# Kernel tuning notes

Measured on AMD Instinct MI355X. Metric: run time of the kernel, lower is better.

The kernel has to match this reference:

```python
import jax, jax.numpy as jnp
import numpy as np

B, S, D = 2, 2048, 2048
H = 16
HD = D // H

def setup_inputs() -> dict:
    key = jax.random.key(0)
    ks = jax.random.split(key, 6)
    s = 1.0 / np.sqrt(D)
    return {
        "inputs": jax.random.normal(ks[0], (B, S, D), dtype=jnp.float32),
        "w_q": jax.random.normal(ks[1], (D, D), dtype=jnp.float32) * s,
        "w_k": jax.random.normal(ks[2], (D, D), dtype=jnp.float32) * s,
        "w_v": jax.random.normal(ks[3], (D, D), dtype=jnp.float32) * s,
        "w_o": jax.random.normal(ks[4], (D, D), dtype=jnp.float32) * s,
        "b_o": jax.random.normal(ks[5], (D,), dtype=jnp.float32) * 0.02,
    }

def reference(inputs, w_q, w_k, w_v, w_o, b_o):
    b, t, _ = inputs.shape
    # Linear layers: y = x @ W^T (weights stored torch-style [out, in])
    q = (inputs @ w_q.T).reshape(b, t, H, HD)
    k = (inputs @ w_k.T).reshape(b, t, H, HD)
    v = (inputs @ w_v.T).reshape(b, t, H, HD)
    # scores: [b, h, t, t]
    scores = jnp.einsum('bqhd,bkhd->bhqk', q, k)
    causal = jnp.triu(jnp.ones((t, t), dtype=bool), k=1)
    scores = jnp.where(causal, -jnp.inf, scores)
    # NOTE: source scales by sqrt(token_num) (keys.shape[2] after transpose), not sqrt(head_dim)
    scale = jnp.float32(t) ** 0.5
    attn = jax.nn.softmax(scores / scale, axis=-1)
    ctx = jnp.einsum('bhqk,bkhd->bqhd', attn, v).reshape(b, t, D)
    return ctx @ w_o.T + b_o
```

## Files before the change

### kernel.cpp

```cpp
#include <hip/hip_runtime.h>


typedef __attribute__((ext_vector_type(8))) short short8;
typedef __attribute__((ext_vector_type(4))) float f32x4;

#define SEQ 2048
#define DM  2048
#define NHD 128
#define NT  32
#define QSCALE (0.022097086912079608f * 1.4426950408889634f)

#define EXP2F(x) __builtin_amdgcn_exp2f(x)
#define WAITV(N) asm volatile("s_waitcnt vmcnt(" #N ")" ::: "memory")

__device__ __forceinline__ unsigned short f2bf(float f) {
  unsigned u = __builtin_bit_cast(unsigned, f);
  u += 0x7FFFu + ((u >> 16) & 1u);
  return (unsigned short)(u >> 16);
}
__device__ __forceinline__ unsigned short f2bf_fast(float f) {
  unsigned u = __builtin_bit_cast(unsigned, f);
  return (unsigned short)((u + 0x8000u) >> 16);
}

__device__ __forceinline__ void gll16(const void* g, void* l) {
  __builtin_amdgcn_global_load_lds((const __attribute__((address_space(1))) void*)g,
                                   (__attribute__((address_space(3))) void*)l, 16, 0, 0);
}

template <int CTRL>
__device__ __forceinline__ float dpp_mv(float x) {
  int xi = __builtin_bit_cast(int, x);
  return __builtin_bit_cast(float,
      __builtin_amdgcn_update_dpp(xi, xi, CTRL, 0xF, 0xF, false));
}
__device__ __forceinline__ float red16_max(float x) {
  x = fmaxf(x, dpp_mv<0xB1>(x));
  x = fmaxf(x, dpp_mv<0x4E>(x));
  x = fmaxf(x, dpp_mv<0x124>(x));
  x = fmaxf(x, dpp_mv<0x128>(x));
  return x;
}
__device__ __forceinline__ float red16_sum(float x) {
  x += dpp_mv<0xB1>(x);
  x += dpp_mv<0x4E>(x);
  x += dpp_mv<0x124>(x);
  x += dpp_mv<0x128>(x);
  return x;
}

__global__ __launch_bounds__(256) void cast_all_k(const float* __restrict__ X,
                                                  const float* __restrict__ Wq,
                                                  const float* __restrict__ Wk,
                                                  const float* __restrict__ Wv,
                                                  const float* __restrict__ Wo,
                                                  unsigned short* __restrict__ Xb,
                                                  unsigned short* __restrict__ Wqb,
                                                  unsigned short* __restrict__ Wkb,
                                                  unsigned short* __restrict__ Wvb,
                                                  unsigned short* __restrict__ Wob) {
  int i = blockIdx.x * 256 + threadIdx.x;
  const float* src;
  unsigned short* dst;
  int j;
  float sc = 1.0f;
  if (i < 1048576) {
    src = X; dst = Xb; j = i;
  } else {
    int k = i - 1048576;
    int r = k >> 19; j = k & 524287;
    src = (r == 0) ? Wq : (r == 1) ? Wk : (r == 2) ? Wv : Wo;
    dst = (r == 0) ? Wqb : (r == 1) ? Wkb : (r == 2) ? Wvb : Wob;
    if (r == 0) sc = QSCALE;
  }
  const f32x4* p = (const f32x4*)src + (size_t)j * 2;
  f32x4 a = p[0], b = p[1];
  short8 o;
  o[0] = (short)f2bf(a[0] * sc); o[1] = (short)f2bf(a[1] * sc);
  o[2] = (short)f2bf(a[2] * sc); o[3] = (short)f2bf(a[3] * sc);
  o[4] = (short)f2bf(b[0] * sc); o[5] = (short)f2bf(b[1] * sc);
  o[6] = (short)f2bf(b[2] * sc); o[7] = (short)f2bf(b[3] * sc);
  *(short8*)(dst + (size_t)j * 8) = o;
}

__device__ __forceinline__ void stage_half(const unsigned short* __restrict__ gbase,
                                           unsigned short* lhalf, int tid) {
#pragma unroll
  for (int c = 0; c < 2; ++c) {
    int G = c * 512 + tid;
    int row = G >> 3, g = G & 7;
    int gs = g ^ (row & 7);
    gll16(gbase + (size_t)row * DM + gs * 8, lhalf + (size_t)G * 8);
  }
}

#define LOADAF(MH)                                                              \
  _Pragma("unroll") for (int mi = 0; mi < 4; ++mi)                              \
    _Pragma("unroll") for (int ks = 0; ks < 2; ++ks) {                          \
      int row = wm * 64 + mi * 16 + lr;                                         \
      af[mi][ks] = *(const short8*)&lA[(MH) * 8192 + row * 64 +                 \
                                       (((ks * 4 + kb) ^ (row & 7)) * 8)];      \
    }

#define PHASE(MH, NH, STG, WV)                                                  \
  {                                                                             \
    const unsigned short* lBh = lB + (NH) * 8192;                               \
    short8 bfr[2][2];                                                           \
    _Pragma("unroll") for (int ni = 0; ni < 2; ++ni)                            \
      _Pragma("unroll") for (int ks = 0; ks < 2; ++ks) {                        \
        int row = wn * 32 + ni * 16 + lr;                                       \
        bfr[ni][ks] = *(const short8*)&lBh[row * 64 + (((ks * 4 + kb) ^ (row & 7)) * 8)]; \
      }                                                                         \
    STG;                                                                        \
    __builtin_amdgcn_s_barrier();                                               \
    __builtin_amdgcn_s_setprio(1);                                              \
    _Pragma("unroll") for (int mi = 0; mi < 4; ++mi)                            \
      _Pragma("unroll") for (int ni = 0; ni < 2; ++ni) {                        \
        acc[MH][NH][mi][ni] = __builtin_amdgcn_mfma_f32_16x16x32_bf16(          \
            af[mi][0], bfr[ni][0], acc[MH][NH][mi][ni], 0, 0, 0);               \
        acc[MH][NH][mi][ni] = __builtin_amdgcn_mfma_f32_16x16x32_bf16(          \
            af[mi][1], bfr[ni][1], acc[MH][NH][mi][ni], 0, 0, 0);               \
      }                                                                         \
    __builtin_amdgcn_s_setprio(0);                                              \
    WV;                                                                         \
    __builtin_amdgcn_s_barrier();                                               \
  }

__device__ __forceinline__ void gemm256_core(const unsigned short* __restrict__ A,
                                             const unsigned short* __restrict__ B,
                                             unsigned short* LA, unsigned short* LB,
                                             f32x4 acc[2][2][4][2], int m0, int n0) {
  const int tid = threadIdx.x;
  const int w = tid >> 6, l = tid & 63;
  const int lr = l & 15, kb = l >> 4;
  const int wm = w >> 2, wn = w & 3;

  stage_half(A + (size_t)m0 * DM, LA, tid);
  stage_half(B + (size_t)n0 * DM, LB, tid);
  stage_half(B + (size_t)n0 * DM + (size_t)128 * DM, LB + 8192, tid);
  stage_half(A + (size_t)m0 * DM + (size_t)128 * DM, LA + 8192, tid);
  WAITV(4);
  __builtin_amdgcn_s_barrier();

#pragma unroll 1
  for (int t = 0; t < NT; ++t) {
    const unsigned short* lA = LA + (t & 1) * 16384;
    const unsigned short* lB = LB + (t & 1) * 16384;
    unsigned short* sA = LA + ((t + 1) & 1) * 16384;
    unsigned short* sB = LB + ((t + 1) & 1) * 16384;
    const unsigned short* gA = A + (size_t)m0 * DM + (t + 1) * 64;
    const unsigned short* gB = B + (size_t)n0 * DM + (t + 1) * 64;
    const bool st = (t + 1 < NT);
    short8 af[4][2];
    LOADAF(0);
    PHASE(0, 0, if (st) stage_half(gA, sA, tid),
                if (st) { WAITV(4); } else { WAITV(2); });
    PHASE(0, 1, if (st) stage_half(gB, sB, tid),
                if (st) { WAITV(4); } else { WAITV(0); });
    LOADAF(1);
    PHASE(1, 0, if (st) stage_half(gB + (size_t)128 * DM, sB + 8192, tid), );
    PHASE(1, 1, if (st) stage_half(gA + (size_t)128 * DM, sA + 8192, tid),
                if (st) { WAITV(4); });
  }
}

__global__ __launch_bounds__(512, 2) void gemm_qk_k(const unsigned short* __restrict__ X,
                                                    const unsigned short* __restrict__ Wq,
                                                    const unsigned short* __restrict__ Wk,
                                                    unsigned short* __restrict__ Qo,
                                                    unsigned short* __restrict__ Ko) {
  __shared__ unsigned short LA[32768];
  __shared__ unsigned short LB[32768];
  const int lin = blockIdx.x + 8 * (blockIdx.y + 16 * blockIdx.z);
  const int c = lin & 7, idx = lin >> 3;
  const int xb = (c & 1) * 4 + ((idx >> 2) & 3);
  const int yb = (c >> 1) * 4 + (idx & 3);
  const int zb = idx >> 4;
  const unsigned short* W = zb ? Wk : Wq;
  unsigned short* Y = zb ? Ko : Qo;
  const int m0 = yb * 256, n0 = xb * 256;
  const int tid = threadIdx.x, w = tid >> 6, l = tid & 63;
  const int lr = l & 15, kb = l >> 4;
  const int wm = w >> 2, wn = w & 3;
  f32x4 acc[2][2][4][2] = {};
  gemm256_core(X, W, LA, LB, acc, m0, n0);
#pragma unroll
  for (int mh = 0; mh < 2; ++mh)
#pragma unroll
    for (int nh = 0; nh < 2; ++nh)
#pragma unroll
      for (int mi = 0; mi < 4; ++mi)
#pragma unroll
        for (int ni = 0; ni < 2; ++ni)
#pragma unroll
          for (int rr = 0; rr < 4; ++rr) {
            int row = m0 + mh * 128 + wm * 64 + mi * 16 + kb * 4 + rr;
            int col = n0 + nh * 128 + wn * 32 + ni * 16 + lr;
            Y[(size_t)row * DM + col] = f2bf(acc[mh][nh][mi][ni][rr]);
          }
}

#define PH2(NH, STG, WV)                                                        \
  {                                                                             \
    const unsigned short* lBh = lB + (NH) * 8192;                               \
    short8 bfr[2][2];                                                           \
    _Pragma("unroll") for (int ni = 0; ni < 2; ++ni)                            \
      _Pragma("unroll") for (int ks = 0; ks < 2; ++ks) {                        \
        int row = wn * 32 + ni * 16 + lr;                                       \
        bfr[ni][ks] = *(const short8*)&lBh[row * 64 + (((ks * 4 + kb) ^ (row & 7)) * 8)]; \
      }                                                                         \
    STG;                                                                        \
    __builtin_amdgcn_s_barrier();                                               \
    __builtin_amdgcn_s_setprio(1);                                              \
    _Pragma("unroll") for (int mi = 0; mi < 4; ++mi)                            \
      _Pragma("unroll") for (int ni = 0; ni < 2; ++ni) {                        \
        acc[NH][mi][ni] = __builtin_amdgcn_mfma_f32_16x16x32_bf16(              \
            af[mi][0], bfr[ni][0], acc[NH][mi][ni], 0, 0, 0);                   \
        acc[NH][mi][ni] = __builtin_amdgcn_mfma_f32_16x16x32_bf16(              \
            af[mi][1], bfr[ni][1], acc[NH][mi][ni], 0, 0, 0);                   \
      }                                                                         \
    __builtin_amdgcn_s_setprio(0);                                              \
    WV;                                                                         \
    __builtin_amdgcn_s_barrier();                                               \
  }

__device__ __forceinline__ void gemm128x256_core(const unsigned short* __restrict__ A,
                                                 const unsigned short* __restrict__ B,
                                                 unsigned short* LA, unsigned short* LB,
                                                 f32x4 acc[2][4][2], int m0, int n0) {
  const int tid = threadIdx.x;
  const int w = tid >> 6, l = tid & 63;
  const int lr = l & 15, kb = l >> 4;
  const int wm = w >> 2, wn = w & 3;

  stage_half(A + (size_t)m0 * DM, LA, tid);
  stage_half(B + (size_t)n0 * DM, LB, tid);
  stage_half(B + (size_t)n0 * DM + (size_t)128 * DM, LB + 8192, tid);
  WAITV(2);
  __builtin_amdgcn_s_barrier();

#pragma unroll 1
  for (int t = 0; t < NT; ++t) {
    const unsigned short* lA = LA + (t & 1) * 8192;
    const unsigned short* lB = LB + (t & 1) * 16384;
    unsigned short* sA = LA + ((t + 1) & 1) * 8192;
    unsigned short* sB = LB + ((t + 1) & 1) * 16384;
    const unsigned short* gA = A + (size_t)m0 * DM + (t + 1) * 64;
    const unsigned short* gB = B + (size_t)n0 * DM + (t + 1) * 64;
    const bool st = (t + 1 < NT);
    short8 af[4][2];
#pragma unroll
    for (int mi = 0; mi < 4; ++mi)
#pragma unroll
      for (int ks = 0; ks < 2; ++ks) {
        int row = wm * 64 + mi * 16 + lr;
        af[mi][ks] = *(const short8*)&lA[row * 64 + (((ks * 4 + kb) ^ (row & 7)) * 8)];
      }
    PH2(0, if (st) stage_half(gA, sA, tid),
           if (st) { WAITV(2); } else { WAITV(0); });
    PH2(1, if (st) { stage_half(gB, sB, tid); stage_half(gB + (size_t)128 * DM, sB + 8192, tid); },
           if (st) { WAITV(2); });
  }
}

__global__ __launch_bounds__(512, 2) void gemm_vt_k(const unsigned short* __restrict__ Wv,
                                                    const unsigned short* __restrict__ X,
                                                    unsigned short* __restrict__ Vt) {
  __shared__ unsigned short LA[16384];
  __shared__ unsigned short LB[32768];
  const int lin = blockIdx.x + 16 * blockIdx.y;
  const int c = lin & 7, idx = lin >> 3;
  const int yb = (c >> 2) * 8 + (idx & 7);
  const int xb = (c & 3) * 4 + (idx >> 3);
  const int m0 = yb * 128, n0 = xb * 256;
  const int tid = threadIdx.x, w = tid >> 6, l = tid & 63;
  const int lr = l & 15, kb = l >> 4;
  const int wm = w >> 2, wn = w & 3;
  f32x4 acc[2][4][2] = {};
  gemm128x256_core(Wv, X, LA, LB, acc, m0, n0);
#pragma unroll
  for (int nh = 0; nh < 2; ++nh)
#pragma unroll
    for (int mi = 0; mi < 4; ++mi)
#pragma unroll
      for (int ni = 0; ni < 2; ++ni)
#pragma unroll
        for (int rr = 0; rr < 4; ++rr) {
          int i = m0 + wm * 64 + mi * 16 + kb * 4 + rr;
          int j = n0 + nh * 128 + wn * 32 + ni * 16 + lr;
          Vt[((size_t)(j >> 11) * 2048 + i) * 2048 + (j & 2047)] = f2bf(acc[nh][mi][ni][rr]);
        }
}

__global__ __launch_bounds__(512, 2) void gemm_o_k(const unsigned short* __restrict__ A,
                                                   const unsigned short* __restrict__ W,
                                                   const float* __restrict__ bias,
                                                   float* __restrict__ Y) {
  __shared__ unsigned short LA[16384];
  __shared__ unsigned short LB[32768];
  const int lin = blockIdx.x + 8 * blockIdx.y;
  const int c = lin & 7, idx = lin >> 3;
  const int yb = (c >> 1) * 8 + (idx & 7);
  const int xb = (c & 1) * 4 + (idx >> 3);
  const int m0 = yb * 128, n0 = xb * 256;
  const int tid = threadIdx.x, w = tid >> 6, l = tid & 63;
  const int lr = l & 15, kb = l >> 4;
  const int wm = w >> 2, wn = w & 3;
  f32x4 acc[2][4][2] = {};
  gemm128x256_core(A, W, LA, LB, acc, m0, n0);
#pragma unroll
  for (int nh = 0; nh < 2; ++nh)
#pragma unroll
    for (int mi = 0; mi < 4; ++mi)
#pragma unroll
      for (int ni = 0; ni < 2; ++ni)
#pragma unroll
        for (int rr = 0; rr < 4; ++rr) {
          int row = m0 + wm * 64 + mi * 16 + kb * 4 + rr;
          int col = n0 + nh * 128 + wn * 32 + ni * 16 + lr;
          Y[(size_t)row * DM + col] = acc[nh][mi][ni][rr] + bias[col];
        }
}

__device__ __forceinline__ void stage_tiles8(const unsigned short* __restrict__ Kh,
                                             const unsigned short* __restrict__ Vh,
                                             unsigned short* KL, unsigned short* VL,
                                             int kv0, int t) {
#pragma unroll
  for (int c = 0; c < 2; ++c) {
    int S = c * 512 + t;
    int row = S >> 4, g = (S & 15) ^ (row & 7);
    gll16(Kh + (size_t)(kv0 + row) * DM + g * 8, KL + (size_t)S * 8);
  }
#pragma unroll
  for (int c = 0; c < 2; ++c) {
    int S = c * 512 + t;
    int d = S >> 3, g = (S & 7) ^ (d & 7);
    gll16(Vh + (size_t)d * SEQ + kv0 + g * 8, VL + (size_t)S * 8);
  }
}

__device__ __forceinline__ void attn_tile(const unsigned short* __restrict__ Kc,
                                          const unsigned short* __restrict__ Vc,
                                          unsigned short* __restrict__ Pw,
                                          const short8 qf[4], f32x4 ctx[8],
                                          float mrow[4], float lpart[4],
                                          int qw, int kv0, int lr, int kb) {
  f32x4 s[4];
  __builtin_amdgcn_s_setprio(1);
#pragma unroll
  for (int ct = 0; ct < 4; ++ct) {
    s[ct] = (f32x4){0.f, 0.f, 0.f, 0.f};
    int krow = ct * 16 + lr;
#pragma unroll
    for (int ks = 0; ks < 4; ++ks) {
      short8 bf = *(const short8*)&Kc[krow * 128 + (((ks * 4 + kb) ^ (krow & 7)) * 8)];
      s[ct] = __builtin_amdgcn_mfma_f32_16x16x32_bf16(qf[ks], bf, s[ct], 0, 0, 0);
    }
  }
  __builtin_amdgcn_s_setprio(0);
  if (kv0 + 63 > qw) {
#pragma unroll
    for (int r = 0; r < 4; ++r) {
      const int qi = qw + kb * 4 + r;
#pragma unroll
      for (int ct = 0; ct < 4; ++ct)
        if (kv0 + ct * 16 + lr > qi) s[ct][r] = -3.0e4f;
    }
  }
  float mxl[4];
#pragma unroll
  for (int r = 0; r < 4; ++r)
    mxl[r] = fmaxf(fmaxf(s[0][r], s[1][r]), fmaxf(s[2][r], s[3][r]));
  bool hit = (mxl[0] > mrow[0] + 8.f) | (mxl[1] > mrow[1] + 8.f) |
             (mxl[2] > mrow[2] + 8.f) | (mxl[3] > mrow[3] + 8.f);
  if (__any(hit)) {
#pragma unroll
    for (int r = 0; r < 4; ++r) {
      float mx = red16_max(mxl[r]);
      if (mx > mrow[r] + 8.f) {
        float alpha = EXP2F(mrow[r] - mx);
        mrow[r] = mx;
        lpart[r] *= alpha;
#pragma unroll
        for (int cc = 0; cc < 8; ++cc) ctx[cc][r] *= alpha;
      }
    }
  }
  float pe[4][4];
#pragma unroll
  for (int r = 0; r < 4; ++r) {
#pragma unroll
    for (int ct = 0; ct < 4; ++ct) {
      float e = EXP2F(s[ct][r] - mrow[r]);
      pe[ct][r] = e;
      lpart[r] += e;
    }
  }
#pragma unroll
  for (int ct = 0; ct < 4; ++ct)
#pragma unroll
    for (int r = 0; r < 4; ++r) {
      int prow = kb * 4 + r;
      int g = (ct * 2 + (lr >> 3)) ^ ((prow >> 1) & 7);
      Pw[prow * 64 + g * 8 + (lr & 7)] = f2bf_fast(pe[ct][r]);
    }
  short8 pa[2];
#pragma unroll
  for (int ks = 0; ks < 2; ++ks)
    pa[ks] = *(const short8*)&Pw[lr * 64 + (((ks * 4 + kb) ^ ((lr >> 1) & 7)) * 8)];
  __builtin_amdgcn_s_setprio(1);
#pragma unroll
  for (int cc = 0; cc < 8; ++cc) {
    int vrow = cc * 16 + lr;
#pragma unroll
    for (int ks = 0; ks < 2; ++ks) {
      short8 vb = *(const short8*)&Vc[vrow * 64 + (((ks * 4 + kb) ^ (vrow & 7)) * 8)];
      ctx[cc] = __builtin_amdgcn_mfma_f32_16x16x32_bf16(pa[ks], vb, ctx[cc], 0, 0, 0);
    }
  }
  __builtin_amdgcn_s_setprio(0);
}

__global__ __launch_bounds__(512) void attn_k(const unsigned short* __restrict__ Q,
                                              const unsigned short* __restrict__ K,
                                              const unsigned short* __restrict__ Vt,
                                              unsigned short* __restrict__ O) {
  __shared__ unsigned short KL[2][64 * 128];
  __shared__ unsigned short VL[2][128 * 64];
  __shared__ unsigned short Pb[8][16 * 64];
  const int t = threadIdx.x, w = t >> 6, l = t & 63;
  const int lr = l & 15, kb = l >> 4;
  const int id = blockIdx.x;
  const int xcd = id & 7, s = id >> 3;
  const int bh = xcd * 4 + (s & 3);
  const int yh = s >> 2;
  const int y = (yh < 8) ? yh : (23 - yh);
  const int b = bh >> 4, h = bh & 15;
  const unsigned short* Kh = K + (size_t)b * SEQ * DM + h * NHD;
  const unsigned short* Vh = Vt + (size_t)bh * NHD * SEQ;

  const int qw = y * 128 + w * 16;
  const int nkt = 2 * y + 2;

  short8 qf[4];
  {
    const unsigned short* qp = Q + (size_t)(b * SEQ + qw + lr) * DM + h * NHD + kb * 8;
#pragma unroll
    for (int ks = 0; ks < 4; ++ks) qf[ks] = *(const short8*)(qp + ks * 32);
  }
  f32x4 ctx[8] = {};
  float mrow[4], lpart[4];
#pragma unroll
  for (int r = 0; r < 4; ++r) { mrow[r] = -3.0e4f; lpart[r] = 0.f; }

  stage_tiles8(Kh, Vh, KL[0], VL[0], 0, t);
  __syncthreads();

  int cbuf = 0;
#pragma unroll 1
  for (int kt = 0; kt < nkt; ++kt) {
    const int kv0 = kt * 64;
    if (kt + 1 < nkt) stage_tiles8(Kh, Vh, KL[cbuf ^ 1], VL[cbuf ^ 1], kv0 + 64, t);
    if (kv0 <= qw + 15)
      attn_tile(KL[cbuf], VL[cbuf], Pb[w], qf, ctx, mrow, lpart, qw, kv0, lr, kb);
    __syncthreads();
    cbuf ^= 1;
  }

#pragma unroll
  for (int r = 0; r < 4; ++r) {
    float inv = 1.f / red16_sum(lpart[r]);
    size_t rowoff = (size_t)(b * SEQ + qw + kb * 4 + r) * DM + h * NHD;
#pragma unroll
    for (int cc = 0; cc < 8; ++cc)
      O[rowoff + cc * 16 + lr] = f2bf_fast(ctx[cc][r] * inv);
  }
}

extern "C" void kernel_launch(void* const* d_in, const int* in_sizes, int n_in,
                              void* d_out, int out_size, void* d_ws, size_t ws_size,
                              hipStream_t stream) {
  const float* X  = (const float*)d_in[0];
  const float* Wq = (const float*)d_in[1];
  const float* Wk = (const float*)d_in[2];
  const float* Wv = (const float*)d_in[3];
  const float* Wo = (const float*)d_in[4];
  const float* bo = (const float*)d_in[5];
  float* out = (float*)d_out;

  unsigned short* ws = (unsigned short*)d_ws;
  unsigned short* Xb  = ws;
  unsigned short* Wqb = ws + 8388608;
  unsigned short* Wkb = ws + 12582912;
  unsigned short* Wvb = ws + 16777216;
  unsigned short* Wob = ws + 20971520;
  unsigned short* Qb  = ws + 25165824;
  unsigned short* Kb  = ws + 33554432;
  unsigned short* Vtb = ws + 41943040;
  unsigned short* Cb  = ws + 50331648;

  cast_all_k<<<12288, 256, 0, stream>>>(X, Wq, Wk, Wv, Wo, Xb, Wqb, Wkb, Wvb, Wob);

  gemm_qk_k<<<dim3(8, 16, 2), 512, 0, stream>>>(Xb, Wqb, Wkb, Qb, Kb);
  gemm_vt_k<<<dim3(16, 16), 512, 0, stream>>>(Wvb, Xb, Vtb);
  attn_k<<<512, 512, 0, stream>>>(Qb, Kb, Vtb, Cb);
  gemm_o_k<<<dim3(8, 32), 512, 0, stream>>>(Cb, Wob, bo, out);
}
```

Measured before the change: 236.2 us.

## Split long causal attention rows into two KV halves with a combine kernel

```diff
diff --git a/kernel.cpp b/kernel.cpp
--- a/kernel.cpp
+++ b/kernel.cpp
@@ -21,6 +21,9 @@
 __device__ __forceinline__ unsigned short f2bf_fast(float f) {
   unsigned u = __builtin_bit_cast(unsigned, f);
   return (unsigned short)((u + 0x8000u) >> 16);
+}
+__device__ __forceinline__ float bf2f(unsigned short u) {
+  return __builtin_bit_cast(float, ((unsigned)u) << 16);
 }
 
 __device__ __forceinline__ void gll16(const void* g, void* l) {
@@ -425,23 +428,31 @@
 __global__ __launch_bounds__(512) void attn_k(const unsigned short* __restrict__ Q,
                                               const unsigned short* __restrict__ K,
                                               const unsigned short* __restrict__ Vt,
-                                              unsigned short* __restrict__ O) {
+                                              unsigned short* __restrict__ O,
+                                              unsigned short* __restrict__ Part) {
   __shared__ unsigned short KL[2][64 * 128];
   __shared__ unsigned short VL[2][128 * 64];
   __shared__ unsigned short Pb[8][16 * 64];
   const int t = threadIdx.x, w = t >> 6, l = t & 63;
   const int lr = l & 15, kb = l >> 4;
   const int id = blockIdx.x;
-  const int xcd = id & 7, s = id >> 3;
-  const int bh = xcd * 4 + (s & 3);
-  const int yh = s >> 2;
-  const int y = (yh < 8) ? yh : (23 - yh);
+  const int xcd = id & 7, u = id >> 3;
+  const int bh = xcd * 4 + (u & 3);
+  const int c = u >> 2;
+  const int g = c / 3, r3 = c % 3;
+  int y, kt0, ktN, half = 0;
+  bool full;
+  if (r3 == 2) { y = 7 - g; kt0 = 0; ktN = 2 * y + 2; full = true; }
+  else {
+    y = 15 - g; full = false; half = r3;
+    if (r3 == 0) { kt0 = 0; ktN = y + 1; }
+    else         { kt0 = y + 1; ktN = 2 * y + 2; }
+  }
   const int b = bh >> 4, h = bh & 15;
   const unsigned short* Kh = K + (size_t)b * SEQ * DM + h * NHD;
   const unsigned short* Vh = Vt + (size_t)bh * NHD * SEQ;
 
   const int qw = y * 128 + w * 16;
-  const int nkt = 2 * y + 2;
 
   short8 qf[4];
   {
@@ -454,28 +465,73 @@
 #pragma unroll
   for (int r = 0; r < 4; ++r) { mrow[r] = -3.0e4f; lpart[r] = 0.f; }
 
-  stage_tiles8(Kh, Vh, KL[0], VL[0], 0, t);
+  stage_tiles8(Kh, Vh, KL[0], VL[0], kt0 * 64, t);
   __syncthreads();
 
   int cbuf = 0;
 #pragma unroll 1
-  for (int kt = 0; kt < nkt; ++kt) {
+  for (int kt = kt0; kt < ktN; ++kt) {
     const int kv0 = kt * 64;
-    if (kt + 1 < nkt) stage_tiles8(Kh, Vh, KL[cbuf ^ 1], VL[cbuf ^ 1], kv0 + 64, t);
+    if (kt + 1 < ktN) stage_tiles8(Kh, Vh, KL[cbuf ^ 1], VL[cbuf ^ 1], kv0 + 64, t);
     if (kv0 <= qw + 15)
       attn_tile(KL[cbuf], VL[cbuf], Pb[w], qf, ctx, mrow, lpart, qw, kv0, lr, kb);
     __syncthreads();
     cbuf ^= 1;
   }
 
-#pragma unroll
-  for (int r = 0; r < 4; ++r) {
-    float inv = 1.f / red16_sum(lpart[r]);
-    size_t rowoff = (size_t)(b * SEQ + qw + kb * 4 + r) * DM + h * NHD;
-#pragma unroll
-    for (int cc = 0; cc < 8; ++cc)
-      O[rowoff + cc * 16 + lr] = f2bf_fast(ctx[cc][r] * inv);
-  }
+  if (full) {
+#pragma unroll
+    for (int r = 0; r < 4; ++r) {
+      float inv = 1.f / red16_sum(lpart[r]);
+      size_t rowoff = (size_t)(b * SEQ + qw + kb * 4 + r) * DM + h * NHD;
+#pragma unroll
+      for (int cc = 0; cc < 8; ++cc)
+        O[rowoff + cc * 16 + lr] = f2bf_fast(ctx[cc][r] * inv);
+    }
+  } else {
+    unsigned short* Pq = Part +
+        ((size_t)((bh * 8 + (y - 8)) * 2 + half) * 128 + w * 16) * 136;
+#pragma unroll
+    for (int r = 0; r < 4; ++r) {
+      float lsum = red16_sum(lpart[r]);
+      unsigned short* prow = Pq + (size_t)(kb * 4 + r) * 136;
+#pragma unroll
+      for (int cc = 0; cc < 8; ++cc)
+        prow[cc * 16 + lr] = f2bf_fast(ctx[cc][r]);
+      if (lr == 0) {
+        *(float*)(prow + 128) = mrow[r];
+        *(float*)(prow + 130) = lsum;
+      }
+    }
+  }
+}
+
+__global__ __launch_bounds__(256) void combine_k(const unsigned short* __restrict__ Part,
+                                                 unsigned short* __restrict__ O) {
+  int i = blockIdx.x * 256 + threadIdx.x;
+  int rg = i >> 4;
+  int cg = (i & 15) * 8;
+  int bh = rg >> 10, rem = rg & 1023;
+  int ys = rem >> 7, row = rem & 127;
+  const unsigned short* p1 = Part + ((size_t)((bh * 8 + ys) * 2 + 0) * 128 + row) * 136;
+  const unsigned short* p2 = p1 + (size_t)128 * 136;
+  float m1 = *(const float*)(p1 + 128), l1 = *(const float*)(p1 + 130);
+  float m2 = *(const float*)(p2 + 128), l2 = *(const float*)(p2 + 130);
+  float m = fmaxf(m1, m2);
+  float a1 = EXP2F(m1 - m), a2 = EXP2F(m2 - m);
+  float inv = 1.f / (l1 * a1 + l2 * a2);
+  a1 *= inv; a2 *= inv;
+  short8 c1 = *(const short8*)(p1 + cg);
+  short8 c2 = *(const short8*)(p2 + cg);
+  int b = bh >> 4, h = bh & 15;
+  size_t off = ((size_t)(b * SEQ + (8 + ys) * 128 + row)) * DM + h * NHD + cg;
+  short8 o;
+#pragma unroll
+  for (int j = 0; j < 8; ++j) {
+    float v = bf2f((unsigned short)c1[j]) * a1 + bf2f((unsigned short)c2[j]) * a2;
+    o[j] = (short)f2bf_fast(v);
+  }
+  *(short8*)(O + off) = o;
 }
 
 extern "C" void kernel_launch(void* const* d_in, const int* in_sizes, int n_in,
@@ -499,11 +555,13 @@
   unsigned short* Kb  = ws + 33554432;
   unsigned short* Vtb = ws + 41943040;
   unsigned short* Cb  = ws + 50331648;
+  unsigned short* Prt = Wqb;
 
   cast_all_k<<<12288, 256, 0, stream>>>(X, Wq, Wk, Wv, Wo, Xb, Wqb, Wkb, Wvb, Wob);
 
   gemm_qk_k<<<dim3(8, 16, 2), 512, 0, stream>>>(Xb, Wqb, Wkb, Qb, Kb);
   gemm_vt_k<<<dim3(16, 16), 512, 0, stream>>>(Wvb, Xb, Vtb);
-  attn_k<<<512, 512, 0, stream>>>(Qb, Kb, Vtb, Cb);
+  attn_k<<<768, 512, 0, stream>>>(Qb, Kb, Vtb, Cb, Prt);
+  combine_k<<<2048, 256, 0, stream>>>(Prt, Cb);
   gemm_o_k<<<dim3(8, 32), 512, 0, stream>>>(Cb, Wob, bo, out);
 }
```

Measured after the change: 248.5 us. 1.05x slower.

## Shrink attention blocks to 64 queries with 32-key tiles and 1024 blocks

Applied to the files above, without the earlier changes.

```diff
diff --git a/kernel.cpp b/kernel.cpp
--- a/kernel.cpp
+++ b/kernel.cpp
@@ -322,34 +322,34 @@
         }
 }
 
-__device__ __forceinline__ void stage_tiles8(const unsigned short* __restrict__ Kh,
+__device__ __forceinline__ void stage_tiles4(const unsigned short* __restrict__ Kh,
                                              const unsigned short* __restrict__ Vh,
                                              unsigned short* KL, unsigned short* VL,
                                              int kv0, int t) {
 #pragma unroll
   for (int c = 0; c < 2; ++c) {
-    int S = c * 512 + t;
+    int S = c * 256 + t;
     int row = S >> 4, g = (S & 15) ^ (row & 7);
     gll16(Kh + (size_t)(kv0 + row) * DM + g * 8, KL + (size_t)S * 8);
   }
 #pragma unroll
   for (int c = 0; c < 2; ++c) {
-    int S = c * 512 + t;
-    int d = S >> 3, g = (S & 7) ^ (d & 7);
+    int S = c * 256 + t;
+    int d = S >> 2, g = (S & 3) ^ (d & 3);
     gll16(Vh + (size_t)d * SEQ + kv0 + g * 8, VL + (size_t)S * 8);
   }
 }
 
-__device__ __forceinline__ void attn_tile(const unsigned short* __restrict__ Kc,
-                                          const unsigned short* __restrict__ Vc,
-                                          unsigned short* __restrict__ Pw,
-                                          const short8 qf[4], f32x4 ctx[8],
-                                          float mrow[4], float lpart[4],
-                                          int qw, int kv0, int lr, int kb) {
-  f32x4 s[4];
+__device__ __forceinline__ void attn_tile32(const unsigned short* __restrict__ Kc,
+                                            const unsigned short* __restrict__ Vc,
+                                            unsigned short* __restrict__ Pw,
+                                            const short8 qf[4], f32x4 ctx[8],
+                                            float mrow[4], float lpart[4],
+                                            int qw, int kv0, int lr, int kb) {
+  f32x4 s[2];
   __builtin_amdgcn_s_setprio(1);
 #pragma unroll
-  for (int ct = 0; ct < 4; ++ct) {
+  for (int ct = 0; ct < 2; ++ct) {
     s[ct] = (f32x4){0.f, 0.f, 0.f, 0.f};
     int krow = ct * 16 + lr;
 #pragma unroll
@@ -359,19 +359,19 @@
     }
   }
   __builtin_amdgcn_s_setprio(0);
-  if (kv0 + 63 > qw) {
+  if (kv0 + 31 > qw) {
 #pragma unroll
     for (int r = 0; r < 4; ++r) {
       const int qi = qw + kb * 4 + r;
 #pragma unroll
-      for (int ct = 0; ct < 4; ++ct)
+      for (int ct = 0; ct < 2; ++ct)
         if (kv0 + ct * 16 + lr > qi) s[ct][r] = -3.0e4f;
     }
   }
   float mxl[4];
 #pragma unroll
   for (int r = 0; r < 4; ++r)
-    mxl[r] = fmaxf(fmaxf(s[0][r], s[1][r]), fmaxf(s[2][r], s[3][r]));
+    mxl[r] = fmaxf(s[0][r], s[1][r]);
   bool hit = (mxl[0] > mrow[0] + 8.f) | (mxl[1] > mrow[1] + 8.f) |
              (mxl[2] > mrow[2] + 8.f) | (mxl[3] > mrow[3] + 8.f);
   if (__any(hit)) {
@@ -387,61 +387,55 @@
       }
     }
   }
-  float pe[4][4];
+  float pe[2][4];
 #pragma unroll
   for (int r = 0; r < 4; ++r) {
 #pragma unroll
-    for (int ct = 0; ct < 4; ++ct) {
+    for (int ct = 0; ct < 2; ++ct) {
       float e = EXP2F(s[ct][r] - mrow[r]);
       pe[ct][r] = e;
       lpart[r] += e;
     }
   }
 #pragma unroll
-  for (int ct = 0; ct < 4; ++ct)
+  for (int ct = 0; ct < 2; ++ct)
 #pragma unroll
     for (int r = 0; r < 4; ++r) {
       int prow = kb * 4 + r;
-      int g = (ct * 2 + (lr >> 3)) ^ ((prow >> 1) & 7);
-      Pw[prow * 64 + g * 8 + (lr & 7)] = f2bf_fast(pe[ct][r]);
+      int gk = ct * 2 + (lr >> 3);
+      Pw[prow * 32 + ((gk ^ (prow & 3)) * 8) + (lr & 7)] = f2bf_fast(pe[ct][r]);
     }
-  short8 pa[2];
-#pragma unroll
-  for (int ks = 0; ks < 2; ++ks)
-    pa[ks] = *(const short8*)&Pw[lr * 64 + (((ks * 4 + kb) ^ ((lr >> 1) & 7)) * 8)];
+  short8 pa = *(const short8*)&Pw[lr * 32 + (((kb ^ (lr & 3)) * 8))];
   __builtin_amdgcn_s_setprio(1);
 #pragma unroll
   for (int cc = 0; cc < 8; ++cc) {
     int vrow = cc * 16 + lr;
-#pragma unroll
-    for (int ks = 0; ks < 2; ++ks) {
-      short8 vb = *(const short8*)&Vc[vrow * 64 + (((ks * 4 + kb) ^ (vrow & 7)) * 8)];
-      ctx[cc] = __builtin_amdgcn_mfma_f32_16x16x32_bf16(pa[ks], vb, ctx[cc], 0, 0, 0);
-    }
+    short8 vb = *(const short8*)&Vc[vrow * 32 + (((kb ^ (vrow & 3)) * 8))];
+    ctx[cc] = __builtin_amdgcn_mfma_f32_16x16x32_bf16(pa, vb, ctx[cc], 0, 0, 0);
   }
   __builtin_amdgcn_s_setprio(0);
 }
 
-__global__ __launch_bounds__(512) void attn_k(const unsigned short* __restrict__ Q,
+__global__ __launch_bounds__(256) void attn_k(const unsigned short* __restrict__ Q,
                                               const unsigned short* __restrict__ K,
                                               const unsigned short* __restrict__ Vt,
                                               unsigned short* __restrict__ O) {
-  __shared__ unsigned short KL[2][64 * 128];
-  __shared__ unsigned short VL[2][128 * 64];
-  __shared__ unsigned short Pb[8][16 * 64];
+  __shared__ unsigned short KL[2][32 * 128];
+  __shared__ unsigned short VL[2][128 * 32];
+  __shared__ unsigned short Pb[4][16 * 32];
   const int t = threadIdx.x, w = t >> 6, l = t & 63;
   const int lr = l & 15, kb = l >> 4;
   const int id = blockIdx.x;
   const int xcd = id & 7, s = id >> 3;
   const int bh = xcd * 4 + (s & 3);
-  const int yh = s >> 2;
-  const int y = (yh < 8) ? yh : (23 - yh);
+  const int xh = s >> 2;
+  const int x = (xh < 16) ? (31 - xh) : (xh - 16);
   const int b = bh >> 4, h = bh & 15;
   const unsigned short* Kh = K + (size_t)b * SEQ * DM + h * NHD;
   const unsigned short* Vh = Vt + (size_t)bh * NHD * SEQ;
 
-  const int qw = y * 128 + w * 16;
-  const int nkt = 2 * y + 2;
+  const int qw = x * 64 + w * 16;
+  const int nkt = 2 * x + 2;
 
   short8 qf[4];
   {
@@ -454,16 +448,16 @@
 #pragma unroll
   for (int r = 0; r < 4; ++r) { mrow[r] = -3.0e4f; lpart[r] = 0.f; }
 
-  stage_tiles8(Kh, Vh, KL[0], VL[0], 0, t);
+  stage_tiles4(Kh, Vh, KL[0], VL[0], 0, t);
   __syncthreads();
 
   int cbuf = 0;
 #pragma unroll 1
   for (int kt = 0; kt < nkt; ++kt) {
-    const int kv0 = kt * 64;
-    if (kt + 1 < nkt) stage_tiles8(Kh, Vh, KL[cbuf ^ 1], VL[cbuf ^ 1], kv0 + 64, t);
+    const int kv0 = kt * 32;
+    if (kt + 1 < nkt) stage_tiles4(Kh, Vh, KL[cbuf ^ 1], VL[cbuf ^ 1], kv0 + 32, t);
     if (kv0 <= qw + 15)
-      attn_tile(KL[cbuf], VL[cbuf], Pb[w], qf, ctx, mrow, lpart, qw, kv0, lr, kb);
+      attn_tile32(KL[cbuf], VL[cbuf], Pb[w], qf, ctx, mrow, lpart, qw, kv0, lr, kb);
     __syncthreads();
     cbuf ^= 1;
   }
@@ -504,6 +498,6 @@
 
   gemm_qk_k<<<dim3(8, 16, 2), 512, 0, stream>>>(Xb, Wqb, Wkb, Qb, Kb);
   gemm_vt_k<<<dim3(16, 16), 512, 0, stream>>>(Wvb, Xb, Vtb);
-  attn_k<<<512, 512, 0, stream>>>(Qb, Kb, Vtb, Cb);
+  attn_k<<<1024, 256, 0, stream>>>(Qb, Kb, Vtb, Cb);
   gemm_o_k<<<dim3(8, 32), 512, 0, stream>>>(Cb, Wob, bo, out);
 }
```

New measurement: 269.3 us. 14.0% more time.
